# Optimization experiments

Measured on AMD Instinct MI355X. Metric: run time of the kernel, lower is better.

The kernel has to match this reference:

```python
import jax, jax.numpy as jnp
import numpy as np

ALPHA = 2.6
OPTIMAL_RANK = 1.0
SIGMA = 1.8


def setup_inputs() -> dict:
    key = jax.random.key(0)
    k1, k2 = jax.random.split(key)
    B, D, NP = 2048, 768, 8
    q_reps = jax.random.normal(k1, (B, D), dtype=jnp.float32)
    p_reps = jax.random.normal(k2, (B * NP, D), dtype=jnp.float32)
    return {"q_reps": q_reps, "p_reps": p_reps, "n_passages": NP}


def reference(q_reps, p_reps, n_passages):
    B = q_reps.shape[0]
    # [B, P] contrastive score matrix
    scores = jnp.matmul(q_reps, p_reps.T)
    target = jnp.arange(B, dtype=jnp.int32) * n_passages

    # rank position of the positive passage per query (descending argsort)
    rankings = jnp.argsort(-scores, axis=1)            # [B, P]
    positive_rankings = jnp.argmax(
        rankings == target[:, None], axis=1
    ).astype(jnp.float32)                              # [B]

    # per-sample cross-entropy (reduction='none')
    logp = jax.nn.log_softmax(scores, axis=1)
    raw_loss = -jnp.take_along_axis(logp, target[:, None], axis=1)[:, 0]

    # Gaussian rank weighting: w = 1 + alpha * exp(-(r - r_opt)^2 / (2 sigma^2))
    extra_weight = jnp.exp(-((positive_rankings - OPTIMAL_RANK) ** 2) / (2.0 * SIGMA ** 2))
    weights = 1.0 + ALPHA * extra_weight

    loss = jnp.mean(raw_loss * weights)
    return loss
```

## Files before the change

kernel.cpp:

```cpp
#include <hip/hip_runtime.h>
#include <math.h>


#define BQ 2048
#define DD 768
#define NPASS 8
#define PP 16384
#define BM 256
#define BN 256
#define BK 128
#define KITERS 6
#define NBLK 64
#define MBLK 8
#define NCHUNKS 256

#define ALPHA_C 2.6f
#define INV_2SIG2 (1.0f/6.48f)

typedef __attribute__((ext_vector_type(4))) float floatx4;

#define NQ8   196608
#define NTOT8 1769472
#define NCB   6912
__global__ __launch_bounds__(256) void prep_kernel(const float* __restrict__ qf,
                                                   const float* __restrict__ pf,
                                                   uint2* __restrict__ qb,
                                                   uint2* __restrict__ pb,
                                                   float* __restrict__ st,
                                                   float* __restrict__ out) {
  const int b = blockIdx.x;
  if (b == 0 && threadIdx.x == 0) *out = 0.f;
  if (b < NCB) {
    const int i = b * 256 + threadIdx.x;
    const float4* src; uint2* dst;
    if (i < NQ8) { src = (const float4*)qf + 2 * (size_t)i; dst = qb + i; }
    else { const size_t j = (size_t)i - NQ8; src = (const float4*)pf + 2 * j; dst = pb + j; }
    const float4 a = src[0], c = src[1];
    unsigned lo = __builtin_amdgcn_cvt_pk_fp8_f32(a.x, a.y, 0, 0);
    lo = __builtin_amdgcn_cvt_pk_fp8_f32(a.z, a.w, lo, 1);
    unsigned hi = __builtin_amdgcn_cvt_pk_fp8_f32(c.x, c.y, 0, 0);
    hi = __builtin_amdgcn_cvt_pk_fp8_f32(c.z, c.w, hi, 1);
    uint2 w; w.x = lo; w.y = hi;
    *dst = w;
  } else {
    const int wv = threadIdx.x >> 6, lane = threadIdx.x & 63;
    const int qi = (b - NCB) * 4 + wv;
    const float4* q4 = (const float4*)(qf + (size_t)qi * DD);
    const float4* p4 = (const float4*)(pf + (size_t)qi * NPASS * DD);
    float acc = 0.f;
#pragma unroll
    for (int u = 0; u < 3; ++u) {
      float4 a = q4[lane + 64 * u];
      float4 c = p4[lane + 64 * u];
      acc = fmaf(a.x, c.x, acc);
      acc = fmaf(a.y, c.y, acc);
      acc = fmaf(a.z, c.z, acc);
      acc = fmaf(a.w, c.w, acc);
    }
#pragma unroll
    for (int off = 32; off >= 1; off >>= 1) acc += __shfl_xor(acc, off);
    if (lane == 0) st[qi] = acc;
  }
}

__global__ __launch_bounds__(1024) void gemm_kernel(const unsigned char* __restrict__ qb,
                                                    const unsigned char* __restrict__ pb,
                                                    const float* __restrict__ st,
                                                    float* __restrict__ pm,
                                                    float* __restrict__ pl,
                                                    float* __restrict__ pc) {
  __shared__ unsigned char As[2][32 * 1024];
  __shared__ unsigned char Bs[2][32 * 1024];
  __shared__ float st_lds[BM];

  const int t = threadIdx.x;
  const int lane = t & 63;
  const int wv = t >> 6;
  const int wm = wv >> 2, wn = wv & 3;
  const int bid = blockIdx.x;
  const int xcd = bid & 7;
  const int nb = xcd * 8 + ((bid >> 3) & 7);
  const int mb = bid >> 6;
  const int qbase = mb * BM;
  const int n0 = nb * BN;
  const int lm = lane & 15;
  const int lq = lane >> 4;
  const int lds_lane = lane * 16;

  if (t < BM) st_lds[t] = st[qbase + t];

  floatx4 acc[4][4];
#pragma unroll
  for (int i = 0; i < 4; ++i)
#pragma unroll
    for (int j = 0; j < 4; ++j) acc[i][j] = (floatx4){0.f, 0.f, 0.f, 0.f};

  const size_t arow = (size_t)(qbase + wv * 16 + lm) * DD;
  const size_t brow = (size_t)(n0 + wv * 16 + lm) * DD;

#define STAGE(KT, BUF)                                                          \
  {                                                                             \
    const size_t koff = (size_t)(KT) * BK + lq * 16;                            \
    _Pragma("unroll")                                                           \
    for (int kh = 0; kh < 2; ++kh) {                                            \
      __builtin_amdgcn_global_load_lds(                                         \
          (const __attribute__((address_space(1))) void*)(qb + arow + koff + kh * 64), \
          (__attribute__((address_space(3))) void*)(&As[BUF][(wv * 2 + kh) * 1024] + lds_lane), \
          16, 0, 0);                                                            \
      __builtin_amdgcn_global_load_lds(                                         \
          (const __attribute__((address_space(1))) void*)(pb + brow + koff + kh * 64), \
          (__attribute__((address_space(3))) void*)(&Bs[BUF][(wv * 2 + kh) * 1024] + lds_lane), \
          16, 0, 0);                                                            \
    }                                                                           \
  }

  STAGE(0, 0)
  for (int kt = 0; kt < KITERS; ++kt) {
    const int cb = kt & 1;
    __syncthreads();
    if (kt < KITERS - 1) STAGE(kt + 1, cb ^ 1)
#pragma unroll
    for (int ks = 0; ks < 4; ++ks) {
      const int kh = ks >> 1;
      const int intra = ((ks & 1) * 2 + (lq >> 1)) * 256 + lm * 16 + (lq & 1) * 8;
      long a[4], b[4];
#pragma unroll
      for (int i = 0; i < 4; ++i)
        a[i] = *(const long*)(&As[cb][((wm * 4 + i) * 2 + kh) * 1024] + intra);
#pragma unroll
      for (int j = 0; j < 4; ++j)
        b[j] = *(const long*)(&Bs[cb][((wn * 4 + j) * 2 + kh) * 1024] + intra);
#pragma unroll
      for (int i = 0; i < 4; ++i)
#pragma unroll
        for (int j = 0; j < 4; ++j)
          acc[i][j] = __builtin_amdgcn_mfma_f32_16x16x32_fp8_fp8(a[i], b[j], acc[i][j], 0, 0, 0);
    }
  }

#pragma unroll
  for (int i = 0; i < 4; ++i) {
#pragma unroll
    for (int r = 0; r < 4; ++r) {
      const int rl = wm * 64 + i * 16 + lq * 4 + r;
      float mx = fmaxf(fmaxf(acc[i][0][r], acc[i][1][r]),
                       fmaxf(acc[i][2][r], acc[i][3][r]));
#pragma unroll
      for (int off = 1; off <= 8; off <<= 1) mx = fmaxf(mx, __shfl_xor(mx, off));
      const float stv = st_lds[rl];
      const int qg = qbase + rl;
      const int tcol = qg * NPASS;
      float sum = 0.f, c = 0.f;
#pragma unroll
      for (int j = 0; j < 4; ++j) {
        const float s = acc[i][j][r];
        sum += __expf(s - mx);
        const int cg = n0 + wn * 64 + j * 16 + lm;
        if (s > stv && cg != tcol) c += 1.f;
      }
#pragma unroll
      for (int off = 1; off <= 8; off <<= 1) {
        sum += __shfl_xor(sum, off);
        c += __shfl_xor(c, off);
      }
      if (lm == 0) {
        const int chunk = nb * 4 + wn;
        const size_t idx = (size_t)qg * NCHUNKS + chunk;
        pm[idx] = mx; pl[idx] = sum; pc[idx] = c;
      }
    }
  }
}

__global__ __launch_bounds__(256) void finalize_kernel(const float* __restrict__ st,
                                                       const float* __restrict__ pm,
                                                       const float* __restrict__ pl,
                                                       const float* __restrict__ pc,
                                                       float* __restrict__ out) {
  const int wv = threadIdx.x >> 6, lane = threadIdx.x & 63;
  const int qi = blockIdx.x * 4 + wv;
  float4 m4 = ((const float4*)(pm + (size_t)qi * NCHUNKS))[lane];
  float mx = fmaxf(fmaxf(m4.x, m4.y), fmaxf(m4.z, m4.w));
#pragma unroll
  for (int off = 32; off >= 1; off >>= 1) mx = fmaxf(mx, __shfl_xor(mx, off));
  float4 l4 = ((const float4*)(pl + (size_t)qi * NCHUNKS))[lane];
  float4 c4 = ((const float4*)(pc + (size_t)qi * NCHUNKS))[lane];
  float l = l4.x * __expf(m4.x - mx) + l4.y * __expf(m4.y - mx) +
            l4.z * __expf(m4.z - mx) + l4.w * __expf(m4.w - mx);
  float c = c4.x + c4.y + c4.z + c4.w;
#pragma unroll
  for (int off = 32; off >= 1; off >>= 1) {
    l += __shfl_xor(l, off);
    c += __shfl_xor(c, off);
  }
  float loss = 0.f;
  if (lane == 0) {
    const float raw = logf(l) + mx - st[qi];
    const float dr = c - 1.0f;
    const float w = 1.0f + ALPHA_C * __expf(-(dr * dr) * INV_2SIG2);
    loss = raw * w * (1.0f / (float)BQ);
  }
  __shared__ float red[4];
  if (lane == 0) red[wv] = loss;
  __syncthreads();
  if (threadIdx.x == 0) atomicAdd(out, red[0] + red[1] + red[2] + red[3]);
}

extern "C" void kernel_launch(void* const* d_in, const int* in_sizes, int n_in,
                              void* d_out, int out_size, void* d_ws, size_t ws_size,
                              hipStream_t stream) {
  const float* q = (const float*)d_in[0];
  const float* p = (const float*)d_in[1];
  char* ws = (char*)d_ws;
  unsigned char* qb = (unsigned char*)ws;
  unsigned char* pb = (unsigned char*)(ws + 1572864);
  float* st = (float*)(ws + 14155776);
  float* pm = (float*)(ws + 14163968);
  float* pl = (float*)(ws + 16261120);
  float* pc = (float*)(ws + 18358272);
  float* out = (float*)d_out;

  prep_kernel<<<NCB + BQ / 4, 256, 0, stream>>>(q, p, (uint2*)qb, (uint2*)pb, st, out);
  gemm_kernel<<<NBLK * MBLK, 1024, 0, stream>>>(qb, pb, st, pm, pl, pc);
  finalize_kernel<<<BQ / 4, 256, 0, stream>>>(st, pm, pl, pc, out);
}
```

Measured before the change: 164.4 us.

## Shrink GEMM tile to 128x256 with 512 threads and transpose partial-stat layout

Halves the M tile and K step of the fp8 GEMM and uses 512-thread blocks with smaller LDS buffers, doubling the block count to 1024 so more blocks can be resident per CU. Partial softmax and rank statistics are now stored chunk-major so the finalize kernel reads them coalesced, one query per lane, with an online max/sum merge. The trade-off is more K iterations and barriers per block and less reuse of each B tile across rows.

Result: slower. 180.9 us (+10.1%).

```diff
diff --git a/kernel.cpp b/kernel.cpp
--- a/kernel.cpp
+++ b/kernel.cpp
@@ -6,12 +6,12 @@
 #define DD 768
 #define NPASS 8
 #define PP 16384
-#define BM 256
+#define BM 128
 #define BN 256
-#define BK 128
-#define KITERS 6
+#define BK 64
+#define KITERS 12
 #define NBLK 64
-#define MBLK 8
+#define MBLK 16
 #define NCHUNKS 256
 
 #define ALPHA_C 2.6f
@@ -63,14 +63,14 @@
   }
 }
 
-__global__ __launch_bounds__(1024) void gemm_kernel(const unsigned char* __restrict__ qb,
-                                                    const unsigned char* __restrict__ pb,
-                                                    const float* __restrict__ st,
-                                                    float* __restrict__ pm,
-                                                    float* __restrict__ pl,
-                                                    float* __restrict__ pc) {
-  __shared__ unsigned char As[2][32 * 1024];
-  __shared__ unsigned char Bs[2][32 * 1024];
+__global__ __launch_bounds__(512) void gemm_kernel(const unsigned char* __restrict__ qb,
+                                                   const unsigned char* __restrict__ pb,
+                                                   const float* __restrict__ st,
+                                                   float* __restrict__ pm,
+                                                   float* __restrict__ pl,
+                                                   float* __restrict__ pc) {
+  __shared__ unsigned char As[2][8 * 1024];
+  __shared__ unsigned char Bs[2][16 * 1024];
   __shared__ float st_lds[BM];
 
   const int t = threadIdx.x;
@@ -96,20 +96,20 @@
     for (int j = 0; j < 4; ++j) acc[i][j] = (floatx4){0.f, 0.f, 0.f, 0.f};
 
   const size_t arow = (size_t)(qbase + wv * 16 + lm) * DD;
-  const size_t brow = (size_t)(n0 + wv * 16 + lm) * DD;
+  const size_t brow = (size_t)(n0 + wv * 32 + lm) * DD;
 
 #define STAGE(KT, BUF)                                                          \
   {                                                                             \
     const size_t koff = (size_t)(KT) * BK + lq * 16;                            \
+    __builtin_amdgcn_global_load_lds(                                           \
+        (const __attribute__((address_space(1))) void*)(qb + arow + koff),      \
+        (__attribute__((address_space(3))) void*)(&As[BUF][wv * 1024] + lds_lane), \
+        16, 0, 0);                                                              \
     _Pragma("unroll")                                                           \
-    for (int kh = 0; kh < 2; ++kh) {                                            \
+    for (int u = 0; u < 2; ++u) {                                               \
       __builtin_amdgcn_global_load_lds(                                         \
-          (const __attribute__((address_space(1))) void*)(qb + arow + koff + kh * 64), \
-          (__attribute__((address_space(3))) void*)(&As[BUF][(wv * 2 + kh) * 1024] + lds_lane), \
-          16, 0, 0);                                                            \
-      __builtin_amdgcn_global_load_lds(                                         \
-          (const __attribute__((address_space(1))) void*)(pb + brow + koff + kh * 64), \
-          (__attribute__((address_space(3))) void*)(&Bs[BUF][(wv * 2 + kh) * 1024] + lds_lane), \
+          (const __attribute__((address_space(1))) void*)(pb + brow + (size_t)u * 16 * DD + koff), \
+          (__attribute__((address_space(3))) void*)(&Bs[BUF][(wv * 2 + u) * 1024] + lds_lane), \
           16, 0, 0);                                                            \
     }                                                                           \
   }
@@ -120,16 +120,15 @@
     __syncthreads();
     if (kt < KITERS - 1) STAGE(kt + 1, cb ^ 1)
 #pragma unroll
-    for (int ks = 0; ks < 4; ++ks) {
-      const int kh = ks >> 1;
-      const int intra = ((ks & 1) * 2 + (lq >> 1)) * 256 + lm * 16 + (lq & 1) * 8;
+    for (int ks = 0; ks < 2; ++ks) {
+      const int intra = (ks * 2 + (lq >> 1)) * 256 + lm * 16 + (lq & 1) * 8;
       long a[4], b[4];
 #pragma unroll
       for (int i = 0; i < 4; ++i)
-        a[i] = *(const long*)(&As[cb][((wm * 4 + i) * 2 + kh) * 1024] + intra);
+        a[i] = *(const long*)(&As[cb][(wm * 4 + i) * 1024] + intra);
 #pragma unroll
       for (int j = 0; j < 4; ++j)
-        b[j] = *(const long*)(&Bs[cb][((wn * 4 + j) * 2 + kh) * 1024] + intra);
+        b[j] = *(const long*)(&Bs[cb][(wn * 4 + j) * 1024] + intra);
 #pragma unroll
       for (int i = 0; i < 4; ++i)
 #pragma unroll
@@ -138,6 +137,10 @@
     }
   }
 
+  const int chunk = nb * 4 + wn;
+  float* const pmc = pm + (size_t)chunk * BQ;
+  float* const plc = pl + (size_t)chunk * BQ;
+  float* const pcc = pc + (size_t)chunk * BQ;
 #pragma unroll
   for (int i = 0; i < 4; ++i) {
 #pragma unroll
@@ -164,9 +167,7 @@
         c += __shfl_xor(c, off);
       }
       if (lm == 0) {
-        const int chunk = nb * 4 + wn;
-        const size_t idx = (size_t)qg * NCHUNKS + chunk;
-        pm[idx] = mx; pl[idx] = sum; pc[idx] = c;
+        pmc[qg] = mx; plc[qg] = sum; pcc[qg] = c;
       }
     }
   }
@@ -178,32 +179,37 @@
                                                        const float* __restrict__ pc,
                                                        float* __restrict__ out) {
   const int wv = threadIdx.x >> 6, lane = threadIdx.x & 63;
-  const int qi = blockIdx.x * 4 + wv;
-  float4 m4 = ((const float4*)(pm + (size_t)qi * NCHUNKS))[lane];
-  float mx = fmaxf(fmaxf(m4.x, m4.y), fmaxf(m4.z, m4.w));
-#pragma unroll
-  for (int off = 32; off >= 1; off >>= 1) mx = fmaxf(mx, __shfl_xor(mx, off));
-  float4 l4 = ((const float4*)(pl + (size_t)qi * NCHUNKS))[lane];
-  float4 c4 = ((const float4*)(pc + (size_t)qi * NCHUNKS))[lane];
-  float l = l4.x * __expf(m4.x - mx) + l4.y * __expf(m4.y - mx) +
-            l4.z * __expf(m4.z - mx) + l4.w * __expf(m4.w - mx);
-  float c = c4.x + c4.y + c4.z + c4.w;
-#pragma unroll
-  for (int off = 32; off >= 1; off >>= 1) {
-    l += __shfl_xor(l, off);
-    c += __shfl_xor(c, off);
-  }
-  float loss = 0.f;
-  if (lane == 0) {
-    const float raw = logf(l) + mx - st[qi];
-    const float dr = c - 1.0f;
+  const int q = blockIdx.x * 64 + lane;
+  const int c0 = wv * 64;
+  float m = -1e30f, l = 0.f, c = 0.f;
+#pragma unroll 4
+  for (int ch = 0; ch < 64; ++ch) {
+    const size_t idx = (size_t)(c0 + ch) * BQ + q;
+    const float mv = pm[idx], lv = pl[idx], cv = pc[idx];
+    const float nm = fmaxf(m, mv);
+    l = l * __expf(m - nm) + lv * __expf(mv - nm);
+    m = nm; c += cv;
+  }
+  __shared__ float sm[4][64], sl[4][64], sc[4][64];
+  sm[wv][lane] = m; sl[wv][lane] = l; sc[wv][lane] = c;
+  __syncthreads();
+  if (wv == 0) {
+    float M = sm[0][lane], L = sl[0][lane], C = sc[0][lane];
+#pragma unroll
+    for (int w = 1; w < 4; ++w) {
+      const float mv = sm[w][lane];
+      const float nm = fmaxf(M, mv);
+      L = L * __expf(M - nm) + sl[w][lane] * __expf(mv - nm);
+      M = nm; C += sc[w][lane];
+    }
+    const float raw = logf(L) + M - st[q];
+    const float dr = C - 1.0f;
     const float w = 1.0f + ALPHA_C * __expf(-(dr * dr) * INV_2SIG2);
-    loss = raw * w * (1.0f / (float)BQ);
-  }
-  __shared__ float red[4];
-  if (lane == 0) red[wv] = loss;
-  __syncthreads();
-  if (threadIdx.x == 0) atomicAdd(out, red[0] + red[1] + red[2] + red[3]);
+    float loss = raw * w * (1.0f / (float)BQ);
+#pragma unroll
+    for (int off = 32; off >= 1; off >>= 1) loss += __shfl_xor(loss, off);
+    if (lane == 0) atomicAdd(out, loss);
+  }
 }
 
 extern "C" void kernel_launch(void* const* d_in, const int* in_sizes, int n_in,
@@ -221,6 +227,6 @@
   float* out = (float*)d_out;
 
   prep_kernel<<<NCB + BQ / 4, 256, 0, stream>>>(q, p, (uint2*)qb, (uint2*)pb, st, out);
-  gemm_kernel<<<NBLK * MBLK, 1024, 0, stream>>>(qb, pb, st, pm, pl, pc);
-  finalize_kernel<<<BQ / 4, 256, 0, stream>>>(st, pm, pl, pc, out);
-}
+  gemm_kernel<<<NBLK * MBLK, 512, 0, stream>>>(qb, pb, st, pm, pl, pc);
+  finalize_kernel<<<BQ / 64, 256, 0, stream>>>(st, pm, pl, pc, out);
+}
```
